# Optimization experiments

Hardware: AMD Instinct MI355X
Metric: run time of the kernel (lower is better)

The kernel has to match this reference:

```python
import jax, jax.numpy as jnp
import numpy as np

N = 30000   # nodes
E = 120000  # edges
G = 512     # graphs in batch
F_IN = 1
H1 = 32
H2 = 64
NC = 10


def _lin_init(key, fan_in, fan_out):
    s = 1.0 / np.sqrt(fan_in)
    kw, kb = jax.random.split(key)
    w = jax.random.uniform(kw, (fan_in, fan_out), jnp.float32, minval=-s, maxval=s)
    b = jax.random.uniform(kb, (fan_out,), jnp.float32, minval=-s, maxval=s)
    return w, b


def setup_inputs() -> dict:
    key = jax.random.key(0)
    ks = jax.random.split(key, 16)
    inp = {}
    inp["x"] = jax.random.normal(ks[0], (N, F_IN), jnp.float32)
    inp["edge_attr"] = jax.random.uniform(ks[1], (E, 2), jnp.float32)
    inp["pos"] = jax.random.uniform(ks[2], (N, 2), jnp.float32) * 27.0
    inp["w1a"], inp["b1a"] = _lin_init(ks[3], 2, 25)
    inp["w1b"], inp["b1b"] = _lin_init(ks[4], 25, F_IN * H1)
    inp["root1"], inp["bias1"] = _lin_init(ks[5], F_IN, H1)
    inp["w2a"], inp["b2a"] = _lin_init(ks[6], 2, 25)
    inp["w2b"], inp["b2b"] = _lin_init(ks[7], 25, H1 * H2)
    inp["root2"], inp["bias2"] = _lin_init(ks[8], H1, H2)
    inp["fc1_w"], inp["fc1_b"] = _lin_init(ks[9], H2, 128)
    inp["fc2_w"], inp["fc2_b"] = _lin_init(ks[10], 128, NC)
    inp["edge_index"] = jax.random.randint(ks[11], (2, E), 0, N)
    inp["batch"] = jnp.sort(jax.random.randint(ks[12], (N,), 0, G))
    return inp


def _seg_mean(v, idx, n):
    s = jax.ops.segment_sum(v, idx, num_segments=n)
    c = jax.ops.segment_sum(jnp.ones((v.shape[0], 1), v.dtype), idx, num_segments=n)
    return s / jnp.maximum(c, 1.0)


def _nnconv(x, src, dst, ea, wa, ba, wb, bb, root, bias, n_seg, n_out):
    # per-edge weight matrix from edge MLP: [E, f_in, f_out]
    f_in, f_out = root.shape
    W = (jax.nn.relu(ea @ wa + ba) @ wb + bb).reshape(-1, f_in, f_out)
    msg = jnp.einsum('ei,eio->eo', x[src], W)          # gather + per-edge matmul
    aggr = _seg_mean(msg, dst, n_seg)[:n_out]          # mean scatter-reduce
    return aggr + x @ root + bias


def _forward(x, edge_attr, pos, w1a, b1a, w1b, b1b, root1, bias1,
             w2a, b2a, w2b, b2b, root2, bias2, fc1_w, fc1_b, fc2_w, fc2_b,
             edge_index, batch):
    row, col = edge_index[0], edge_index[1]
    h = jax.nn.elu(_nnconv(x, row, col, edge_attr, w1a, b1a, w1b, b1b,
                           root1, bias1, N, N))
    # graclus stand-in: fixed pairwise matching (consecutive cluster ids)
    n2 = N // 2
    cluster1 = jnp.arange(N) // 2
    x2 = jax.ops.segment_max(h, cluster1, num_segments=n2)     # max_pool x
    pos2 = _seg_mean(pos, cluster1, n2)                        # pool_pos (mean)
    batch2 = batch[0::2]                                       # pool_batch via perm
    row2 = cluster1[row]
    col2 = cluster1[col]
    mask = row2 != col2                                        # drop self loops
    col2m = jnp.where(mask, col2, n2)                          # route to dummy seg
    cart = (pos2[col2] - pos2[row2]) * mask[:, None]           # cartesian pseudo
    max_v = jnp.abs(cart).max()
    ea2 = cart / (2.0 * max_v) + 0.5
    h2 = jax.nn.elu(_nnconv(x2, row2, col2m, ea2, w2a, b2a, w2b, b2b,
                            root2, bias2, n2 + 1, n2))
    n3 = n2 // 2
    cluster2 = jnp.arange(n2) // 2
    x3 = jax.ops.segment_max(h2, cluster2, num_segments=n3)    # max_pool_x
    batch3 = batch2[0::2]
    g = _seg_mean(x3, batch3, G)                               # global_mean_pool
    g = jax.nn.elu(g @ fc1_w + fc1_b)                          # dropout off (eval)
    return jax.nn.log_softmax(g @ fc2_w + fc2_b, axis=1)


def reference(x, edge_attr, pos, w1a, b1a, w1b, b1b, root1, bias1,
              w2a, b2a, w2b, b2b, root2, bias2, fc1_w, fc1_b, fc2_w, fc2_b,
              edge_index, batch):
    return _forward(x, edge_attr, pos, w1a, b1a, w1b, b1b, root1, bias1,
                    w2a, b2a, w2b, b2b, root2, bias2, fc1_w, fc1_b,
                    fc2_w, fc2_b, edge_index, batch)
```

## Files before the change

kernel.cpp:

```cpp
#include <hip/hip_runtime.h>
#include <hip/hip_bf16.h>

#define N_NODES 30000
#define N_EDGES 120000
#define NGRAPH  512
#define N2      15000
#define N3      7500
#define NC      10

#define TSN   4
#define NTS   (N2 / TSN)
#define EC4   64
#define NB1   32
#define NBLK1 ((N_NODES + NB1 - 1) / NB1)
#define EC1   128

#define SC_C1 118
#define SC_C2 59
#define SC_CS 15
#define SC_CT (SC_C1 + SC_C2 + SC_CS)

typedef __hip_bfloat16 bf16;

__device__ __forceinline__ float lo(const float* p, int i) { return p[i]; }
__device__ __forceinline__ float lo(const bf16* p, int i) { return __bfloat162float(p[i]); }
__device__ __forceinline__ void sto(float* p, int i, float v) { p[i] = v; }
__device__ __forceinline__ void sto(bf16* p, int i, float v) { p[i] = __float2bfloat16(v); }
__device__ __forceinline__ float elu(float x) { return x > 0.f ? x : expm1f(x); }
template <typename T> __host__ __device__ constexpr int want_flag() { return sizeof(T) == 4 ? 1 : 0; }

#define MV_OFF    0
#define GS_OFF    1
#define GC_OFF    32769
#define DEG1_OFF  33281
#define DEG2_OFF  63281
#define DEGS_OFF  78281
#define ZERO_FLOATS 82031
#define OFF1_OFF  82031
#define CUR1_OFF  112032
#define OFF2_OFF  142032
#define CUR2_OFF  157033
#define OFFS_OFF  172033
#define CURS_OFF  175784
#define BSUM_OFF  179534
#define ES1_OFF   179726
#define ESS_OFF   299726
#define DPOS_OFF  419726
#define X2_OFF    539726
#define P2_OFF    1019726
#define CT_OFF    1049726
#define H2_OFF    1289726
#define MSG_OFF   2249726
#define FLAG_OFF  9929726

__global__ __launch_bounds__(256) void k0_detect(const void* x, const void* ea, int* flag) {
  const bf16* xb = (const bf16*)x;
  const bf16* eb = (const bf16*)ea;
  int tid = threadIdx.x;
  float a = __bfloat162float(xb[tid]);
  float b = __bfloat162float(eb[tid]);
  int bad = (!(fabsf(a) < 1e3f)) || (!(fabsf(b) < 1e3f));
  unsigned long long m = __ballot(bad);
  __shared__ int anyb[4];
  int w = tid >> 6;
  if ((tid & 63) == 0) anyb[w] = (m != 0ULL) ? 1 : 0;
  __syncthreads();
  if (tid == 0) flag[0] = (anyb[0] | anyb[1] | anyb[2] | anyb[3]);
}

__global__ __launch_bounds__(256) void kc_deg(const int* __restrict__ ei,
                                              int* __restrict__ deg1,
                                              int* __restrict__ deg2,
                                              int* __restrict__ degS) {
  int e = blockIdx.x * 256 + threadIdx.x;
  if (e >= N_EDGES) return;
  int row = ei[e], col = ei[N_EDGES + e];
  atomicAdd(deg1 + col, 1);
  int r2 = row >> 1, c2 = col >> 1;
  if (r2 != c2) {
    atomicAdd(deg2 + c2, 1);
    atomicAdd(degS + (r2 >> 2), 1);
  }
}

__global__ __launch_bounds__(256) void ks_scanA(
    const int* __restrict__ deg1, const int* __restrict__ deg2, const int* __restrict__ degS,
    int* __restrict__ off1, int* __restrict__ off2, int* __restrict__ offS,
    int* __restrict__ bsum) {
  __shared__ int buf[256];
  int c = blockIdx.x, tid = threadIdx.x;
  const int* deg; int* off; int n, local;
  if (c < SC_C1)              { deg = deg1; off = off1; n = 30000; local = c; }
  else if (c < SC_C1 + SC_C2) { deg = deg2; off = off2; n = 15000; local = c - SC_C1; }
  else                        { deg = degS; off = offS; n = 3750;  local = c - SC_C1 - SC_C2; }
  int i = local * 256 + tid;
  int v = (i < n) ? deg[i] : 0;
  buf[tid] = v;
  __syncthreads();
  for (int s = 1; s < 256; s <<= 1) {
    int t = (tid >= s) ? buf[tid - s] : 0;
    __syncthreads();
    buf[tid] += t;
    __syncthreads();
  }
  if (i <= n) off[i] = buf[tid] - v;
  if (tid == 255) bsum[c] = buf[255];
}

__global__ __launch_bounds__(256) void ks_scanB(int* __restrict__ bsum) {
  __shared__ int buf[256];
  int a = blockIdx.x, tid = threadIdx.x;
  int nc, cb;
  if (a == 0)      { nc = SC_C1; cb = 0; }
  else if (a == 1) { nc = SC_C2; cb = SC_C1; }
  else             { nc = SC_CS; cb = SC_C1 + SC_C2; }
  int v = (tid < nc) ? bsum[cb + tid] : 0;
  buf[tid] = v;
  __syncthreads();
  for (int s = 1; s < 256; s <<= 1) {
    int t = (tid >= s) ? buf[tid - s] : 0;
    __syncthreads();
    buf[tid] += t;
    __syncthreads();
  }
  if (tid < nc) bsum[cb + tid] = buf[tid] - v;
}

__global__ __launch_bounds__(256) void ks_scanC(
    int* __restrict__ off1, int* __restrict__ off2, int* __restrict__ offS,
    int* __restrict__ cur1, int* __restrict__ cur2, int* __restrict__ curS,
    const int* __restrict__ bsum) {
  int c = blockIdx.x, tid = threadIdx.x;
  int* off; int* cur; int n, local;
  if (c < SC_C1)              { off = off1; cur = cur1; n = 30000; local = c; }
  else if (c < SC_C1 + SC_C2) { off = off2; cur = cur2; n = 15000; local = c - SC_C1; }
  else                        { off = offS; cur = curS; n = 3750;  local = c - SC_C1 - SC_C2; }
  int add = bsum[c];
  int i = local * 256 + tid;
  if (i <= n) off[i] += add;
  if (i < n) cur[i] = off[i];
}

__global__ __launch_bounds__(256) void kc_place(const int* __restrict__ ei,
                                                int* __restrict__ cur1, int* __restrict__ es1,
                                                int* __restrict__ cur2, int* __restrict__ dpos,
                                                int* __restrict__ curS, int* __restrict__ ess) {
  int e = blockIdx.x * 256 + threadIdx.x;
  if (e >= N_EDGES) return;
  int row = ei[e], col = ei[N_EDGES + e];
  int p = atomicAdd(cur1 + col, 1);
  es1[p] = e;
  int r2 = row >> 1, c2 = col >> 1;
  if (r2 != c2) {
    int q = atomicAdd(cur2 + c2, 1);
    dpos[e] = q;
    int u = atomicAdd(curS + (r2 >> 2), 1);
    ess[u] = e;
  }
}

template <typename T>
__global__ __launch_bounds__(256, 4) void k1_blk(
    const int* __restrict__ flag,
    const T* __restrict__ x, const T* __restrict__ ea, const T* __restrict__ pos,
    const int* __restrict__ ei,
    const T* __restrict__ w1a, const T* __restrict__ b1a,
    const T* __restrict__ w1b, const T* __restrict__ b1b,
    const T* __restrict__ root1, const T* __restrict__ bias1,
    const int* __restrict__ off1, const int* __restrict__ es1,
    float* __restrict__ x2, float* __restrict__ pos2) {
  if (flag[0] != want_flag<T>()) return;
  __shared__ float w1a_l[50];
  __shared__ float b1a_l[25];
  __shared__ float w1b_l[800];
  __shared__ float b1b_l[32];
  __shared__ float r1_l[32];
  __shared__ float bs1_l[32];
  __shared__ float tl2[25][EC1];
  __shared__ float xsl[EC1];
  __shared__ float hbuf[NB1][33];
  __shared__ int offl[NB1 + 1];
  int tid = threadIdx.x, t = blockIdx.x;
  int n0 = t * NB1;
  for (int j = tid; j < 50; j += 256) w1a_l[j] = lo(w1a, j);
  for (int j = tid; j < 25; j += 256) b1a_l[j] = lo(b1a, j);
  for (int j = tid; j < 800; j += 256) w1b_l[j] = lo(w1b, j);
  if (tid < 32) {
    b1b_l[tid] = lo(b1b, tid);
    r1_l[tid] = lo(root1, tid);
    bs1_l[tid] = lo(bias1, tid);
  }
  if (tid <= NB1) {
    int n = n0 + tid; if (n > N_NODES) n = N_NODES;
    offl[tid] = off1[n];
  }
  __syncthreads();
  int jbeg = offl[0], jend = offl[NB1];
  int wv = tid >> 6, lane = tid & 63, o = lane & 31, hf = lane >> 5;
  float acc[8];
#pragma unroll
  for (int s = 0; s < 8; ++s) acc[s] = 0.f;
  for (int jb = jbeg; jb < jend; jb += EC1) {
    int ecnt = jend - jb; if (ecnt > EC1) ecnt = EC1;
    __syncthreads();
    if (tid < ecnt) {
      int e = es1[jb + tid];
      float a0 = lo(ea, 2 * e), a1 = lo(ea, 2 * e + 1);
      xsl[tid] = lo(x, ei[e]);
#pragma unroll
      for (int k = 0; k < 25; ++k)
        tl2[k][tid] = fmaxf(a0 * w1a_l[k] + a1 * w1a_l[25 + k] + b1a_l[k], 0.f);
    }
    __syncthreads();
#pragma unroll
    for (int s = 0; s < 8; ++s) {
      int nl = wv + 4 * s;
      int lj = offl[nl]; if (lj < jb) lj = jb;
      int hj = offl[nl + 1]; if (hj > jb + ecnt) hj = jb + ecnt;
      for (int j = lj + hf; j < hj; j += 2) {
        int sj = j - jb;
        float macc = b1b_l[o];
#pragma unroll
        for (int k = 0; k < 25; ++k) macc += tl2[k][sj] * w1b_l[k * 32 + o];
        acc[s] += xsl[sj] * macc;
      }
    }
  }
#pragma unroll
  for (int s = 0; s < 8; ++s) {
    int nl = wv + 4 * s;
    float a = acc[s] + __shfl_xor(acc[s], 32, 64);
    int n = n0 + nl;
    if (hf == 0 && n < N_NODES) {
      float c = (float)(offl[nl + 1] - offl[nl]);
      c = fmaxf(c, 1.f);
      hbuf[nl][o] = elu(a / c + lo(x, n) * r1_l[o] + bs1_l[o]);
    }
  }
  __syncthreads();
  for (int idx = tid; idx < (NB1 / 2) * 32; idx += 256) {
    int pl = idx >> 5, oo = idx & 31;
    int m = t * (NB1 / 2) + pl;
    if (m < N2)
      x2[m * 32 + oo] = fmaxf(hbuf[2 * pl][oo], hbuf[2 * pl + 1][oo]);
  }
  if (tid < NB1) {
    int pl = tid >> 1, c = tid & 1;
    int m = t * (NB1 / 2) + pl;
    if (m < N2)
      pos2[m * 2 + c] = 0.5f * (lo(pos, (2 * m) * 2 + c) + lo(pos, (2 * m + 1) * 2 + c));
  }
}

__global__ __launch_bounds__(256) void k3_cart(
    const int* __restrict__ ei, const float* __restrict__ pos2,
    float* __restrict__ cart, unsigned int* __restrict__ maxv) {
  int e = blockIdx.x * 256 + threadIdx.x;
  float m = 0.f;
  if (e < N_EDGES) {
    int r2 = ei[e] >> 1, c2 = ei[N_EDGES + e] >> 1;
    float cx = 0.f, cy = 0.f;
    if (r2 != c2) {
      cx = pos2[2 * c2] - pos2[2 * r2];
      cy = pos2[2 * c2 + 1] - pos2[2 * r2 + 1];
    }
    cart[2 * e] = cx;
    cart[2 * e + 1] = cy;
    m = fmaxf(fabsf(cx), fabsf(cy));
  }
#pragma unroll
  for (int s = 32; s > 0; s >>= 1)
    m = fmaxf(m, __shfl_xor(m, s, 64));
  __shared__ float wm[4];
  int lane = threadIdx.x & 63, wid = threadIdx.x >> 6;
  if (lane == 0) wm[wid] = m;
  __syncthreads();
  if (threadIdx.x == 0) {
    float mm = fmaxf(fmaxf(wm[0], wm[1]), fmaxf(wm[2], wm[3]));
    atomicMax(maxv, __float_as_uint(mm));
  }
}

template <typename T>
__global__ __launch_bounds__(256, 3) void k4_src(
    const int* __restrict__ flag,
    const int* __restrict__ ei, const float* __restrict__ cart, const float* __restrict__ maxv_f,
    const float* __restrict__ x2,
    const T* __restrict__ w2a, const T* __restrict__ b2a,
    const T* __restrict__ w2b, const T* __restrict__ b2b,
    const int* __restrict__ offS, const int* __restrict__ ess,
    const int* __restrict__ dpos,
    float* __restrict__ msg) {
  if (flag[0] != want_flag<T>()) return;
  __shared__ float Y[TSN][26][64];
  __shared__ float xl[TSN][32];
  __shared__ float w2a_l[50];
  __shared__ float b2a_l[25];
  __shared__ __align__(16) float tl[EC4][28];
  __shared__ int dpl[EC4];
  __shared__ int nll[EC4];
  __shared__ float axl[EC4], ayl[EC4];
  int tid = threadIdx.x, t = blockIdx.x;
  int n0 = t * TSN;
  if (tid < TSN * 32) xl[tid >> 5][tid & 31] = x2[n0 * 32 + tid];
  for (int j = tid; j < 50; j += 256) w2a_l[j] = lo(w2a, j);
  for (int j = tid; j < 25; j += 256) b2a_l[j] = lo(b2a, j);
  __syncthreads();
  int w = tid >> 6, o = tid & 63;
  for (int kk = w; kk < 26; kk += 4) {
    const T* srcp = (kk < 25) ? (w2b + kk * 2048) : b2b;
    float a0 = 0.f, a1 = 0.f, a2 = 0.f, a3 = 0.f;
#pragma unroll 8
    for (int i = 0; i < 32; ++i) {
      float q = lo(srcp, i * 64 + o);
      a0 += xl[0][i] * q;
      a1 += xl[1][i] * q;
      a2 += xl[2][i] * q;
      a3 += xl[3][i] * q;
    }
    Y[0][kk][o] = a0; Y[1][kk][o] = a1; Y[2][kk][o] = a2; Y[3][kk][o] = a3;
  }
  float inv = 0.5f / maxv_f[0];
  int j0 = offS[t], j1 = offS[t + 1];
  for (int jb = j0; jb < j1; jb += EC4) {
    int ecnt = j1 - jb; if (ecnt > EC4) ecnt = EC4;
    __syncthreads();
    if (tid < ecnt) {
      int e = ess[jb + tid];
      int r2 = ei[e] >> 1;
      nll[tid] = r2 & (TSN - 1);
      dpl[tid] = dpos[e];
      axl[tid] = cart[2 * e] * inv + 0.5f;
      ayl[tid] = cart[2 * e + 1] * inv + 0.5f;
    }
    __syncthreads();
    for (int idx = tid; idx < ecnt * 32; idx += 256) {
      int j = idx >> 5, k = idx & 31;
      if (k < 25)
        tl[j][k] = fmaxf(axl[j] * w2a_l[k] + ayl[j] * w2a_l[25 + k] + b2a_l[k], 0.f);
    }
    __syncthreads();
    for (int j = w; j < ecnt; j += 4) {
      const float* Yp = &Y[nll[j]][0][0];
      const float* tp = tl[j];
      float acc0 = Yp[25 * 64 + o], acc1 = 0.f, acc2 = 0.f, acc3 = 0.f;
#pragma unroll
      for (int k = 0; k < 24; k += 4) {
        acc0 += tp[k]     * Yp[k * 64 + o];
        acc1 += tp[k + 1] * Yp[(k + 1) * 64 + o];
        acc2 += tp[k + 2] * Yp[(k + 2) * 64 + o];
        acc3 += tp[k + 3] * Yp[(k + 3) * 64 + o];
      }
      acc0 += tp[24] * Yp[24 * 64 + o];
      msg[(size_t)dpl[j] * 64 + o] = (acc0 + acc1) + (acc2 + acc3);
    }
  }
}

template <typename T>
__global__ __launch_bounds__(256) void k5_gather(
    const int* __restrict__ flag,
    const float* __restrict__ msg, const int* __restrict__ off2,
    const float* __restrict__ x2,
    const T* __restrict__ root2, const T* __restrict__ bias2,
    float* __restrict__ h2) {
  if (flag[0] != want_flag<T>()) return;
  __shared__ float r2_l[2048];
  __shared__ float b2_l[64];
  int tid = threadIdx.x;
  for (int j = tid; j < 2048; j += 256) r2_l[j] = lo(root2, j);
  if (tid < 64) b2_l[tid] = lo(bias2, tid);
  __syncthreads();
  int d = blockIdx.x * 4 + (tid >> 6);
  int o = tid & 63;
  int j0 = off2[d], j1 = off2[d + 1];
  float s0 = 0.f, s1 = 0.f;
  int j = j0;
  for (; j + 1 < j1; j += 2) {
    s0 += msg[(size_t)j * 64 + o];
    s1 += msg[(size_t)(j + 1) * 64 + o];
  }
  if (j < j1) s0 += msg[(size_t)j * 64 + o];
  float c = fmaxf((float)(j1 - j0), 1.f);
  float r = b2_l[o];
  const float* xr = x2 + d * 32;
#pragma unroll 8
  for (int i = 0; i < 32; ++i) r += xr[i] * r2_l[i * 64 + o];
  h2[d * 64 + o] = elu((s0 + s1) / c + r);
}

#define K6CH 16
__global__ __launch_bounds__(256) void k6_pool2(
    const float* __restrict__ h2, const int* __restrict__ batch,
    float* __restrict__ gsum, float* __restrict__ gcnt) {
  int wid = blockIdx.x * 4 + (threadIdx.x >> 6);
  int lane = threadIdx.x & 63;
  int m0 = wid * K6CH;
  if (m0 >= N3) return;
  int m1 = m0 + K6CH < N3 ? m0 + K6CH : N3;
  int bcur = batch[4 * m0];
  float acc = 0.f, cnt = 0.f;
  for (int m = m0; m < m1; ++m) {
    int b = batch[4 * m];
    float v = fmaxf(h2[(2 * m) * 64 + lane], h2[(2 * m + 1) * 64 + lane]);
    if (b != bcur) {
      atomicAdd(gsum + bcur * 64 + lane, acc);
      if (lane == 0) atomicAdd(gcnt + bcur, cnt);
      acc = 0.f; cnt = 0.f; bcur = b;
    }
    acc += v; cnt += 1.f;
  }
  atomicAdd(gsum + bcur * 64 + lane, acc);
  if (lane == 0) atomicAdd(gcnt + bcur, cnt);
}

template <typename T>
__global__ __launch_bounds__(128) void k7_head(
    const int* __restrict__ flag,
    const float* __restrict__ gsum, const float* __restrict__ gcnt,
    const T* __restrict__ fc1_w, const T* __restrict__ fc1_b,
    const T* __restrict__ fc2_w, const T* __restrict__ fc2_b,
    T* __restrict__ out) {
  if (flag[0] != want_flag<T>()) return;
  __shared__ float gv[64];
  __shared__ float h1s[128];
  __shared__ float zs[NC];
  __shared__ float lse;
  int g = blockIdx.x, tid = threadIdx.x;
  if (tid < 64) gv[tid] = gsum[g * 64 + tid] / fmaxf(gcnt[g], 1.f);
  __syncthreads();
  float a = lo(fc1_b, tid);
#pragma unroll 8
  for (int o = 0; o < 64; ++o) a += gv[o] * lo(fc1_w, o * 128 + tid);
  h1s[tid] = elu(a);
  __syncthreads();
  if (tid < NC) {
    float s = lo(fc2_b, tid);
    for (int j = 0; j < 128; ++j) s += h1s[j] * lo(fc2_w, j * NC + tid);
    zs[tid] = s;
  }
  __syncthreads();
  if (tid == 0) {
    float m = -1e30f;
    for (int c = 0; c < NC; ++c) m = fmaxf(m, zs[c]);
    float s = 0.f;
    for (int c = 0; c < NC; ++c) s += expf(zs[c] - m);
    lse = m + logf(s);
  }
  __syncthreads();
  if (tid < NC) sto(out, g * NC + tid, zs[tid] - lse);
}

template <typename T>
static void run_conv1(void* const* d_in, float* ws, hipStream_t stream) {
  const int* ei   = (const int*)d_in[19];
  const int* flag = (const int*)(ws + FLAG_OFF);
  k1_blk<T><<<NBLK1, 256, 0, stream>>>(
      flag, (const T*)d_in[0], (const T*)d_in[1], (const T*)d_in[2], ei,
      (const T*)d_in[3], (const T*)d_in[4], (const T*)d_in[5], (const T*)d_in[6],
      (const T*)d_in[7], (const T*)d_in[8],
      (const int*)(ws + OFF1_OFF), (const int*)(ws + ES1_OFF),
      ws + X2_OFF, ws + P2_OFF);
}

template <typename T>
static void run_conv2(void* const* d_in, float* ws, hipStream_t stream) {
  const int* ei   = (const int*)d_in[19];
  const int* flag = (const int*)(ws + FLAG_OFF);
  k4_src<T><<<NTS, 256, 0, stream>>>(
      flag, ei, ws + CT_OFF, ws + MV_OFF, ws + X2_OFF,
      (const T*)d_in[9], (const T*)d_in[10], (const T*)d_in[11], (const T*)d_in[12],
      (const int*)(ws + OFFS_OFF), (const int*)(ws + ESS_OFF),
      (const int*)(ws + DPOS_OFF), ws + MSG_OFF);
  k5_gather<T><<<N2 / 4, 256, 0, stream>>>(
      flag, ws + MSG_OFF, (const int*)(ws + OFF2_OFF), ws + X2_OFF,
      (const T*)d_in[13], (const T*)d_in[14], ws + H2_OFF);
}

extern "C" void kernel_launch(void* const* d_in, const int* in_sizes, int n_in,
                              void* d_out, int out_size, void* d_ws, size_t ws_size,
                              hipStream_t stream) {
  float* ws = (float*)d_ws;
  const int* flag = (const int*)(ws + FLAG_OFF);
  const int* ei = (const int*)d_in[19];
  const int* batch = (const int*)d_in[20];

  k0_detect<<<1, 256, 0, stream>>>(d_in[0], d_in[1], (int*)(ws + FLAG_OFF));
  hipMemsetAsync(d_ws, 0, (size_t)ZERO_FLOATS * 4, stream);

  kc_deg<<<(N_EDGES + 255) / 256, 256, 0, stream>>>(
      ei, (int*)(ws + DEG1_OFF), (int*)(ws + DEG2_OFF), (int*)(ws + DEGS_OFF));
  ks_scanA<<<SC_CT, 256, 0, stream>>>(
      (const int*)(ws + DEG1_OFF), (const int*)(ws + DEG2_OFF), (const int*)(ws + DEGS_OFF),
      (int*)(ws + OFF1_OFF), (int*)(ws + OFF2_OFF), (int*)(ws + OFFS_OFF),
      (int*)(ws + BSUM_OFF));
  ks_scanB<<<3, 256, 0, stream>>>((int*)(ws + BSUM_OFF));
  ks_scanC<<<SC_CT, 256, 0, stream>>>(
      (int*)(ws + OFF1_OFF), (int*)(ws + OFF2_OFF), (int*)(ws + OFFS_OFF),
      (int*)(ws + CUR1_OFF), (int*)(ws + CUR2_OFF), (int*)(ws + CURS_OFF),
      (const int*)(ws + BSUM_OFF));
  kc_place<<<(N_EDGES + 255) / 256, 256, 0, stream>>>(
      ei, (int*)(ws + CUR1_OFF), (int*)(ws + ES1_OFF),
      (int*)(ws + CUR2_OFF), (int*)(ws + DPOS_OFF),
      (int*)(ws + CURS_OFF), (int*)(ws + ESS_OFF));

  run_conv1<float>(d_in, ws, stream);
  run_conv1<bf16>(d_in, ws, stream);

  k3_cart<<<(N_EDGES + 255) / 256, 256, 0, stream>>>(
      ei, ws + P2_OFF, ws + CT_OFF, (unsigned int*)(ws + MV_OFF));

  run_conv2<float>(d_in, ws, stream);
  run_conv2<bf16>(d_in, ws, stream);

  k6_pool2<<<(N3 / K6CH + 4) / 4, 256, 0, stream>>>(
      ws + H2_OFF, batch, ws + GS_OFF, ws + GC_OFF);
  k7_head<float><<<NGRAPH, 128, 0, stream>>>(
      flag, ws + GS_OFF, ws + GC_OFF,
      (const float*)d_in[15], (const float*)d_in[16],
      (const float*)d_in[17], (const float*)d_in[18], (float*)d_out);
  k7_head<bf16><<<NGRAPH, 128, 0, stream>>>(
      flag, ws + GS_OFF, ws + GC_OFF,
      (const bf16*)d_in[15], (const bf16*)d_in[16],
      (const bf16*)d_in[17], (const bf16*)d_in[18], (bf16*)d_out);
}
```

Before: 283.6 us.

## Merge dtype-specialized kernels, fuse pooling into conv2 gather, vectorize per-edge matmuls

```diff
diff --git a/kernel.cpp b/kernel.cpp
--- a/kernel.cpp
+++ b/kernel.cpp
@@ -14,6 +14,7 @@
 #define NB1   32
 #define NBLK1 ((N_NODES + NB1 - 1) / NB1)
 #define EC1   128
+#define NDEGB ((N_EDGES + 255) / 256)
 
 #define SC_C1 118
 #define SC_C2 59
@@ -27,7 +28,6 @@
 __device__ __forceinline__ void sto(float* p, int i, float v) { p[i] = v; }
 __device__ __forceinline__ void sto(bf16* p, int i, float v) { p[i] = __float2bfloat16(v); }
 __device__ __forceinline__ float elu(float x) { return x > 0.f ? x : expm1f(x); }
-template <typename T> __host__ __device__ constexpr int want_flag() { return sizeof(T) == 4 ? 1 : 0; }
 
 #define MV_OFF    0
 #define GS_OFF    1
@@ -49,29 +49,57 @@
 #define X2_OFF    539726
 #define P2_OFF    1019726
 #define CT_OFF    1049726
-#define H2_OFF    1289726
-#define MSG_OFF   2249726
-#define FLAG_OFF  9929726
-
-__global__ __launch_bounds__(256) void k0_detect(const void* x, const void* ea, int* flag) {
-  const bf16* xb = (const bf16*)x;
-  const bf16* eb = (const bf16*)ea;
-  int tid = threadIdx.x;
-  float a = __bfloat162float(xb[tid]);
-  float b = __bfloat162float(eb[tid]);
-  int bad = (!(fabsf(a) < 1e3f)) || (!(fabsf(b) < 1e3f));
-  unsigned long long m = __ballot(bad);
-  __shared__ int anyb[4];
-  int w = tid >> 6;
-  if ((tid & 63) == 0) anyb[w] = (m != 0ULL) ? 1 : 0;
-  __syncthreads();
-  if (tid == 0) flag[0] = (anyb[0] | anyb[1] | anyb[2] | anyb[3]);
-}
-
-__global__ __launch_bounds__(256) void kc_deg(const int* __restrict__ ei,
-                                              int* __restrict__ deg1,
-                                              int* __restrict__ deg2,
-                                              int* __restrict__ degS) {
+#define MSG_OFF   1289726
+#define FLAG_OFF  8969726
+
+struct K1Smem {
+  float tl2[EC1][28];
+  float axl[EC1], ayl[EC1];
+  float xsl[EC1];
+  float w1a[50];
+  float b1a[25];
+  float b1b[32];
+  float r1[32];
+  float bs1[32];
+  float hbuf[NB1][33];
+  int offl[NB1 + 1];
+};
+
+struct K4Smem {
+  float YT[TSN][64][36];
+  float tl[EC4][28];
+  float xl[TSN][32];
+  float w2a[50];
+  float b2a[25];
+  float axl[EC4], ayl[EC4];
+  int dpl[EC4];
+  int nll[EC4];
+};
+
+struct K5Smem {
+  float r2l[2048];
+  float b2l[64];
+  float hl[4][64];
+};
+
+__global__ __launch_bounds__(256) void kc_deg(
+    const int* __restrict__ ei, const void* x, const void* ea, int* __restrict__ flag,
+    int* __restrict__ deg1, int* __restrict__ deg2, int* __restrict__ degS) {
+  if (blockIdx.x == NDEGB) {
+    const bf16* xb = (const bf16*)x;
+    const bf16* eb = (const bf16*)ea;
+    int tid = threadIdx.x;
+    float a = __bfloat162float(xb[tid]);
+    float b = __bfloat162float(eb[tid]);
+    int bad = (!(fabsf(a) < 1e3f)) || (!(fabsf(b) < 1e3f));
+    unsigned long long m = __ballot(bad);
+    __shared__ int anyb[4];
+    int w = tid >> 6;
+    if ((tid & 63) == 0) anyb[w] = (m != 0ULL) ? 1 : 0;
+    __syncthreads();
+    if (tid == 0) flag[0] = (anyb[0] | anyb[1] | anyb[2] | anyb[3]);
+    return;
+  }
   int e = blockIdx.x * 256 + threadIdx.x;
   if (e >= N_EDGES) return;
   int row = ei[e], col = ei[N_EDGES + e];
@@ -160,8 +188,7 @@
 }
 
 template <typename T>
-__global__ __launch_bounds__(256, 4) void k1_blk(
-    const int* __restrict__ flag,
+__device__ void k1_impl(K1Smem& S,
     const T* __restrict__ x, const T* __restrict__ ea, const T* __restrict__ pos,
     const int* __restrict__ ei,
     const T* __restrict__ w1a, const T* __restrict__ b1a,
@@ -169,34 +196,27 @@
     const T* __restrict__ root1, const T* __restrict__ bias1,
     const int* __restrict__ off1, const int* __restrict__ es1,
     float* __restrict__ x2, float* __restrict__ pos2) {
-  if (flag[0] != want_flag<T>()) return;
-  __shared__ float w1a_l[50];
-  __shared__ float b1a_l[25];
-  __shared__ float w1b_l[800];
-  __shared__ float b1b_l[32];
-  __shared__ float r1_l[32];
-  __shared__ float bs1_l[32];
-  __shared__ float tl2[25][EC1];
-  __shared__ float xsl[EC1];
-  __shared__ float hbuf[NB1][33];
-  __shared__ int offl[NB1 + 1];
   int tid = threadIdx.x, t = blockIdx.x;
   int n0 = t * NB1;
-  for (int j = tid; j < 50; j += 256) w1a_l[j] = lo(w1a, j);
-  for (int j = tid; j < 25; j += 256) b1a_l[j] = lo(b1a, j);
-  for (int j = tid; j < 800; j += 256) w1b_l[j] = lo(w1b, j);
+  for (int j = tid; j < 50; j += 256) S.w1a[j] = lo(w1a, j);
+  for (int j = tid; j < 25; j += 256) S.b1a[j] = lo(b1a, j);
   if (tid < 32) {
-    b1b_l[tid] = lo(b1b, tid);
-    r1_l[tid] = lo(root1, tid);
-    bs1_l[tid] = lo(bias1, tid);
+    S.b1b[tid] = lo(b1b, tid);
+    S.r1[tid] = lo(root1, tid);
+    S.bs1[tid] = lo(bias1, tid);
   }
   if (tid <= NB1) {
     int n = n0 + tid; if (n > N_NODES) n = N_NODES;
-    offl[tid] = off1[n];
-  }
-  __syncthreads();
-  int jbeg = offl[0], jend = offl[NB1];
+    S.offl[tid] = off1[n];
+  }
   int wv = tid >> 6, lane = tid & 63, o = lane & 31, hf = lane >> 5;
+  float wreg[28];
+#pragma unroll
+  for (int k = 0; k < 25; ++k) wreg[k] = lo(w1b, k * 32 + o);
+  wreg[25] = wreg[26] = wreg[27] = 0.f;
+  __syncthreads();
+  int jbeg = S.offl[0], jend = S.offl[NB1];
+  float bb = S.b1b[o];
   float acc[8];
 #pragma unroll
   for (int s = 0; s < 8; ++s) acc[s] = 0.f;
@@ -205,24 +225,37 @@
     __syncthreads();
     if (tid < ecnt) {
       int e = es1[jb + tid];
-      float a0 = lo(ea, 2 * e), a1 = lo(ea, 2 * e + 1);
-      xsl[tid] = lo(x, ei[e]);
-#pragma unroll
-      for (int k = 0; k < 25; ++k)
-        tl2[k][tid] = fmaxf(a0 * w1a_l[k] + a1 * w1a_l[25 + k] + b1a_l[k], 0.f);
+      S.axl[tid] = lo(ea, 2 * e);
+      S.ayl[tid] = lo(ea, 2 * e + 1);
+      S.xsl[tid] = lo(x, ei[e]);
+    }
+    __syncthreads();
+    for (int idx = tid; idx < ecnt * 32; idx += 256) {
+      int j = idx >> 5, k = idx & 31;
+      if (k < 25)
+        S.tl2[j][k] = fmaxf(S.axl[j] * S.w1a[k] + S.ayl[j] * S.w1a[25 + k] + S.b1a[k], 0.f);
+      else if (k < 28)
+        S.tl2[j][k] = 0.f;
     }
     __syncthreads();
 #pragma unroll
     for (int s = 0; s < 8; ++s) {
       int nl = wv + 4 * s;
-      int lj = offl[nl]; if (lj < jb) lj = jb;
-      int hj = offl[nl + 1]; if (hj > jb + ecnt) hj = jb + ecnt;
+      int lj = S.offl[nl]; if (lj < jb) lj = jb;
+      int hj = S.offl[nl + 1]; if (hj > jb + ecnt) hj = jb + ecnt;
       for (int j = lj + hf; j < hj; j += 2) {
         int sj = j - jb;
-        float macc = b1b_l[o];
-#pragma unroll
-        for (int k = 0; k < 25; ++k) macc += tl2[k][sj] * w1b_l[k * 32 + o];
-        acc[s] += xsl[sj] * macc;
+        const float4* tq4 = (const float4*)S.tl2[sj];
+        float m0 = bb, m1 = 0.f, m2 = 0.f, m3 = 0.f;
+#pragma unroll
+        for (int q = 0; q < 7; ++q) {
+          float4 tv = tq4[q];
+          m0 += tv.x * wreg[4 * q];
+          m1 += tv.y * wreg[4 * q + 1];
+          m2 += tv.z * wreg[4 * q + 2];
+          m3 += tv.w * wreg[4 * q + 3];
+        }
+        acc[s] += S.xsl[sj] * ((m0 + m1) + (m2 + m3));
       }
     }
   }
@@ -232,9 +265,9 @@
     float a = acc[s] + __shfl_xor(acc[s], 32, 64);
     int n = n0 + nl;
     if (hf == 0 && n < N_NODES) {
-      float c = (float)(offl[nl + 1] - offl[nl]);
+      float c = (float)(S.offl[nl + 1] - S.offl[nl]);
       c = fmaxf(c, 1.f);
-      hbuf[nl][o] = elu(a / c + lo(x, n) * r1_l[o] + bs1_l[o]);
+      S.hbuf[nl][o] = elu(a / c + lo(x, n) * S.r1[o] + S.bs1[o]);
     }
   }
   __syncthreads();
@@ -242,7 +275,7 @@
     int pl = idx >> 5, oo = idx & 31;
     int m = t * (NB1 / 2) + pl;
     if (m < N2)
-      x2[m * 32 + oo] = fmaxf(hbuf[2 * pl][oo], hbuf[2 * pl + 1][oo]);
+      x2[m * 32 + oo] = fmaxf(S.hbuf[2 * pl][oo], S.hbuf[2 * pl + 1][oo]);
   }
   if (tid < NB1) {
     int pl = tid >> 1, c = tid & 1;
@@ -250,6 +283,24 @@
     if (m < N2)
       pos2[m * 2 + c] = 0.5f * (lo(pos, (2 * m) * 2 + c) + lo(pos, (2 * m + 1) * 2 + c));
   }
+}
+
+__global__ __launch_bounds__(256, 4) void k1_both(
+    const int* __restrict__ flag,
+    const void* x, const void* ea, const void* pos, const int* ei,
+    const void* w1a, const void* b1a, const void* w1b, const void* b1b,
+    const void* root1, const void* bias1,
+    const int* off1, const int* es1, float* x2, float* pos2) {
+  extern __shared__ char sm1[];
+  K1Smem& S = *reinterpret_cast<K1Smem*>(sm1);
+  if (flag[0] == 1)
+    k1_impl<float>(S, (const float*)x, (const float*)ea, (const float*)pos, ei,
+                   (const float*)w1a, (const float*)b1a, (const float*)w1b, (const float*)b1b,
+                   (const float*)root1, (const float*)bias1, off1, es1, x2, pos2);
+  else
+    k1_impl<bf16>(S, (const bf16*)x, (const bf16*)ea, (const bf16*)pos, ei,
+                  (const bf16*)w1a, (const bf16*)b1a, (const bf16*)w1b, (const bf16*)b1b,
+                  (const bf16*)root1, (const bf16*)bias1, off1, es1, x2, pos2);
 }
 
 __global__ __launch_bounds__(256) void k3_cart(
@@ -282,43 +333,35 @@
 }
 
 template <typename T>
-__global__ __launch_bounds__(256, 3) void k4_src(
-    const int* __restrict__ flag,
+__device__ void k4_impl(K4Smem& S,
     const int* __restrict__ ei, const float* __restrict__ cart, const float* __restrict__ maxv_f,
     const float* __restrict__ x2,
     const T* __restrict__ w2a, const T* __restrict__ b2a,
     const T* __restrict__ w2b, const T* __restrict__ b2b,
     const int* __restrict__ offS, const int* __restrict__ ess,
-    const int* __restrict__ dpos,
-    float* __restrict__ msg) {
-  if (flag[0] != want_flag<T>()) return;
-  __shared__ float Y[TSN][26][64];
-  __shared__ float xl[TSN][32];
-  __shared__ float w2a_l[50];
-  __shared__ float b2a_l[25];
-  __shared__ __align__(16) float tl[EC4][28];
-  __shared__ int dpl[EC4];
-  __shared__ int nll[EC4];
-  __shared__ float axl[EC4], ayl[EC4];
+    const int* __restrict__ dpos, float* __restrict__ msg) {
   int tid = threadIdx.x, t = blockIdx.x;
   int n0 = t * TSN;
-  if (tid < TSN * 32) xl[tid >> 5][tid & 31] = x2[n0 * 32 + tid];
-  for (int j = tid; j < 50; j += 256) w2a_l[j] = lo(w2a, j);
-  for (int j = tid; j < 25; j += 256) b2a_l[j] = lo(b2a, j);
+  if (tid < TSN * 32) S.xl[tid >> 5][tid & 31] = x2[n0 * 32 + tid];
+  for (int j = tid; j < 50; j += 256) S.w2a[j] = lo(w2a, j);
+  for (int j = tid; j < 25; j += 256) S.b2a[j] = lo(b2a, j);
   __syncthreads();
   int w = tid >> 6, o = tid & 63;
-  for (int kk = w; kk < 26; kk += 4) {
-    const T* srcp = (kk < 25) ? (w2b + kk * 2048) : b2b;
+  for (int kk = w; kk < 28; kk += 4) {
     float a0 = 0.f, a1 = 0.f, a2 = 0.f, a3 = 0.f;
+    if (kk < 26) {
+      const T* srcp = (kk < 25) ? (w2b + kk * 2048) : b2b;
 #pragma unroll 8
-    for (int i = 0; i < 32; ++i) {
-      float q = lo(srcp, i * 64 + o);
-      a0 += xl[0][i] * q;
-      a1 += xl[1][i] * q;
-      a2 += xl[2][i] * q;
-      a3 += xl[3][i] * q;
-    }
-    Y[0][kk][o] = a0; Y[1][kk][o] = a1; Y[2][kk][o] = a2; Y[3][kk][o] = a3;
+      for (int i = 0; i < 32; ++i) {
+        float q = lo(srcp, i * 64 + o);
+        a0 += S.xl[0][i] * q;
+        a1 += S.xl[1][i] * q;
+        a2 += S.xl[2][i] * q;
+        a3 += S.xl[3][i] * q;
+      }
+    }
+    S.YT[0][o][kk] = a0; S.YT[1][o][kk] = a1;
+    S.YT[2][o][kk] = a2; S.YT[3][o][kk] = a3;
   }
   float inv = 0.5f / maxv_f[0];
   int j0 = offS[t], j1 = offS[t + 1];
@@ -328,51 +371,63 @@
     if (tid < ecnt) {
       int e = ess[jb + tid];
       int r2 = ei[e] >> 1;
-      nll[tid] = r2 & (TSN - 1);
-      dpl[tid] = dpos[e];
-      axl[tid] = cart[2 * e] * inv + 0.5f;
-      ayl[tid] = cart[2 * e + 1] * inv + 0.5f;
+      S.nll[tid] = r2 & (TSN - 1);
+      S.dpl[tid] = dpos[e];
+      S.axl[tid] = cart[2 * e] * inv + 0.5f;
+      S.ayl[tid] = cart[2 * e + 1] * inv + 0.5f;
     }
     __syncthreads();
     for (int idx = tid; idx < ecnt * 32; idx += 256) {
       int j = idx >> 5, k = idx & 31;
       if (k < 25)
-        tl[j][k] = fmaxf(axl[j] * w2a_l[k] + ayl[j] * w2a_l[25 + k] + b2a_l[k], 0.f);
+        S.tl[j][k] = fmaxf(S.axl[j] * S.w2a[k] + S.ayl[j] * S.w2a[25 + k] + S.b2a[k], 0.f);
+      else if (k < 28)
+        S.tl[j][k] = (k == 25) ? 1.f : 0.f;
     }
     __syncthreads();
     for (int j = w; j < ecnt; j += 4) {
-      const float* Yp = &Y[nll[j]][0][0];
-      const float* tp = tl[j];
-      float acc0 = Yp[25 * 64 + o], acc1 = 0.f, acc2 = 0.f, acc3 = 0.f;
-#pragma unroll
-      for (int k = 0; k < 24; k += 4) {
-        acc0 += tp[k]     * Yp[k * 64 + o];
-        acc1 += tp[k + 1] * Yp[(k + 1) * 64 + o];
-        acc2 += tp[k + 2] * Yp[(k + 2) * 64 + o];
-        acc3 += tp[k + 3] * Yp[(k + 3) * 64 + o];
+      const float4* yq = (const float4*)&S.YT[S.nll[j]][o][0];
+      const float4* tq = (const float4*)S.tl[j];
+      float a0 = 0.f, a1 = 0.f, a2 = 0.f, a3 = 0.f;
+#pragma unroll
+      for (int q = 0; q < 7; ++q) {
+        float4 tv = tq[q], yv = yq[q];
+        a0 += tv.x * yv.x; a1 += tv.y * yv.y;
+        a2 += tv.z * yv.z; a3 += tv.w * yv.w;
       }
-      acc0 += tp[24] * Yp[24 * 64 + o];
-      msg[(size_t)dpl[j] * 64 + o] = (acc0 + acc1) + (acc2 + acc3);
-    }
-  }
+      msg[(size_t)S.dpl[j] * 64 + o] = (a0 + a1) + (a2 + a3);
+    }
+  }
+}
+
+__global__ __launch_bounds__(256, 3) void k4_both(
+    const int* __restrict__ flag,
+    const int* ei, const float* cart, const float* maxv_f, const float* x2,
+    const void* w2a, const void* b2a, const void* w2b, const void* b2b,
+    const int* offS, const int* ess, const int* dpos, float* msg) {
+  extern __shared__ char sm4[];
+  K4Smem& S = *reinterpret_cast<K4Smem*>(sm4);
+  if (flag[0] == 1)
+    k4_impl<float>(S, ei, cart, maxv_f, x2, (const float*)w2a, (const float*)b2a,
+                   (const float*)w2b, (const float*)b2b, offS, ess, dpos, msg);
+  else
+    k4_impl<bf16>(S, ei, cart, maxv_f, x2, (const bf16*)w2a, (const bf16*)b2a,
+                  (const bf16*)w2b, (const bf16*)b2b, offS, ess, dpos, msg);
 }
 
 template <typename T>
-__global__ __launch_bounds__(256) void k5_gather(
-    const int* __restrict__ flag,
+__device__ void k5_impl(K5Smem& S,
     const float* __restrict__ msg, const int* __restrict__ off2,
     const float* __restrict__ x2,
     const T* __restrict__ root2, const T* __restrict__ bias2,
-    float* __restrict__ h2) {
-  if (flag[0] != want_flag<T>()) return;
-  __shared__ float r2_l[2048];
-  __shared__ float b2_l[64];
+    const int* __restrict__ batch,
+    float* __restrict__ gsum, float* __restrict__ gcnt) {
   int tid = threadIdx.x;
-  for (int j = tid; j < 2048; j += 256) r2_l[j] = lo(root2, j);
-  if (tid < 64) b2_l[tid] = lo(bias2, tid);
-  __syncthreads();
-  int d = blockIdx.x * 4 + (tid >> 6);
-  int o = tid & 63;
+  for (int j = tid; j < 2048; j += 256) S.r2l[j] = lo(root2, j);
+  if (tid < 64) S.b2l[tid] = lo(bias2, tid);
+  __syncthreads();
+  int w = tid >> 6, o = tid & 63;
+  int d = blockIdx.x * 4 + w;
   int j0 = off2[d], j1 = off2[d + 1];
   float s0 = 0.f, s1 = 0.f;
   int j = j0;
@@ -382,46 +437,40 @@
   }
   if (j < j1) s0 += msg[(size_t)j * 64 + o];
   float c = fmaxf((float)(j1 - j0), 1.f);
-  float r = b2_l[o];
+  float r = S.b2l[o];
   const float* xr = x2 + d * 32;
 #pragma unroll 8
-  for (int i = 0; i < 32; ++i) r += xr[i] * r2_l[i * 64 + o];
-  h2[d * 64 + o] = elu((s0 + s1) / c + r);
-}
-
-#define K6CH 16
-__global__ __launch_bounds__(256) void k6_pool2(
-    const float* __restrict__ h2, const int* __restrict__ batch,
-    float* __restrict__ gsum, float* __restrict__ gcnt) {
-  int wid = blockIdx.x * 4 + (threadIdx.x >> 6);
-  int lane = threadIdx.x & 63;
-  int m0 = wid * K6CH;
-  if (m0 >= N3) return;
-  int m1 = m0 + K6CH < N3 ? m0 + K6CH : N3;
-  int bcur = batch[4 * m0];
-  float acc = 0.f, cnt = 0.f;
-  for (int m = m0; m < m1; ++m) {
-    int b = batch[4 * m];
-    float v = fmaxf(h2[(2 * m) * 64 + lane], h2[(2 * m + 1) * 64 + lane]);
-    if (b != bcur) {
-      atomicAdd(gsum + bcur * 64 + lane, acc);
-      if (lane == 0) atomicAdd(gcnt + bcur, cnt);
-      acc = 0.f; cnt = 0.f; bcur = b;
-    }
-    acc += v; cnt += 1.f;
-  }
-  atomicAdd(gsum + bcur * 64 + lane, acc);
-  if (lane == 0) atomicAdd(gcnt + bcur, cnt);
+  for (int i = 0; i < 32; ++i) r += xr[i] * S.r2l[i * 64 + o];
+  S.hl[w][o] = elu((s0 + s1) / c + r);
+  __syncthreads();
+  if (tid < 128) {
+    int p = tid >> 6, oo = tid & 63;
+    float v = fmaxf(S.hl[2 * p][oo], S.hl[2 * p + 1][oo]);
+    int m = blockIdx.x * 2 + p;
+    int g = batch[4 * m];
+    atomicAdd(gsum + g * 64 + oo, v);
+    if (oo == 0) atomicAdd(gcnt + g, 1.f);
+  }
+}
+
+__global__ __launch_bounds__(256) void k5_both(
+    const int* __restrict__ flag,
+    const float* msg, const int* off2, const float* x2,
+    const void* root2, const void* bias2, const int* batch,
+    float* gsum, float* gcnt) {
+  extern __shared__ char sm5[];
+  K5Smem& S = *reinterpret_cast<K5Smem*>(sm5);
+  if (flag[0] == 1)
+    k5_impl<float>(S, msg, off2, x2, (const float*)root2, (const float*)bias2, batch, gsum, gcnt);
+  else
+    k5_impl<bf16>(S, msg, off2, x2, (const bf16*)root2, (const bf16*)bias2, batch, gsum, gcnt);
 }
 
 template <typename T>
-__global__ __launch_bounds__(128) void k7_head(
-    const int* __restrict__ flag,
-    const float* __restrict__ gsum, const float* __restrict__ gcnt,
-    const T* __restrict__ fc1_w, const T* __restrict__ fc1_b,
-    const T* __restrict__ fc2_w, const T* __restrict__ fc2_b,
-    T* __restrict__ out) {
-  if (flag[0] != want_flag<T>()) return;
+__device__ void k7_impl(const float* __restrict__ gsum, const float* __restrict__ gcnt,
+                        const T* __restrict__ fc1_w, const T* __restrict__ fc1_b,
+                        const T* __restrict__ fc2_w, const T* __restrict__ fc2_b,
+                        T* __restrict__ out) {
   __shared__ float gv[64];
   __shared__ float h1s[128];
   __shared__ float zs[NC];
@@ -451,30 +500,17 @@
   if (tid < NC) sto(out, g * NC + tid, zs[tid] - lse);
 }
 
-template <typename T>
-static void run_conv1(void* const* d_in, float* ws, hipStream_t stream) {
-  const int* ei   = (const int*)d_in[19];
-  const int* flag = (const int*)(ws + FLAG_OFF);
-  k1_blk<T><<<NBLK1, 256, 0, stream>>>(
-      flag, (const T*)d_in[0], (const T*)d_in[1], (const T*)d_in[2], ei,
-      (const T*)d_in[3], (const T*)d_in[4], (const T*)d_in[5], (const T*)d_in[6],
-      (const T*)d_in[7], (const T*)d_in[8],
-      (const int*)(ws + OFF1_OFF), (const int*)(ws + ES1_OFF),
-      ws + X2_OFF, ws + P2_OFF);
-}
-
-template <typename T>
-static void run_conv2(void* const* d_in, float* ws, hipStream_t stream) {
-  const int* ei   = (const int*)d_in[19];
-  const int* flag = (const int*)(ws + FLAG_OFF);
-  k4_src<T><<<NTS, 256, 0, stream>>>(
-      flag, ei, ws + CT_OFF, ws + MV_OFF, ws + X2_OFF,
-      (const T*)d_in[9], (const T*)d_in[10], (const T*)d_in[11], (const T*)d_in[12],
-      (const int*)(ws + OFFS_OFF), (const int*)(ws + ESS_OFF),
-      (const int*)(ws + DPOS_OFF), ws + MSG_OFF);
-  k5_gather<T><<<N2 / 4, 256, 0, stream>>>(
-      flag, ws + MSG_OFF, (const int*)(ws + OFF2_OFF), ws + X2_OFF,
-      (const T*)d_in[13], (const T*)d_in[14], ws + H2_OFF);
+__global__ __launch_bounds__(128) void k7_both(
+    const int* __restrict__ flag,
+    const float* gsum, const float* gcnt,
+    const void* fc1_w, const void* fc1_b, const void* fc2_w, const void* fc2_b,
+    void* out) {
+  if (flag[0] == 1)
+    k7_impl<float>(gsum, gcnt, (const float*)fc1_w, (const float*)fc1_b,
+                   (const float*)fc2_w, (const float*)fc2_b, (float*)out);
+  else
+    k7_impl<bf16>(gsum, gcnt, (const bf16*)fc1_w, (const bf16*)fc1_b,
+                  (const bf16*)fc2_w, (const bf16*)fc2_b, (bf16*)out);
 }
 
 extern "C" void kernel_launch(void* const* d_in, const int* in_sizes, int n_in,
@@ -485,11 +521,11 @@
   const int* ei = (const int*)d_in[19];
   const int* batch = (const int*)d_in[20];
 
-  k0_detect<<<1, 256, 0, stream>>>(d_in[0], d_in[1], (int*)(ws + FLAG_OFF));
   hipMemsetAsync(d_ws, 0, (size_t)ZERO_FLOATS * 4, stream);
 
-  kc_deg<<<(N_EDGES + 255) / 256, 256, 0, stream>>>(
-      ei, (int*)(ws + DEG1_OFF), (int*)(ws + DEG2_OFF), (int*)(ws + DEGS_OFF));
+  kc_deg<<<NDEGB + 1, 256, 0, stream>>>(
+      ei, d_in[0], d_in[1], (int*)(ws + FLAG_OFF),
+      (int*)(ws + DEG1_OFF), (int*)(ws + DEG2_OFF), (int*)(ws + DEGS_OFF));
   ks_scanA<<<SC_CT, 256, 0, stream>>>(
       (const int*)(ws + DEG1_OFF), (const int*)(ws + DEG2_OFF), (const int*)(ws + DEGS_OFF),
       (int*)(ws + OFF1_OFF), (int*)(ws + OFF2_OFF), (int*)(ws + OFFS_OFF),
@@ -499,28 +535,31 @@
       (int*)(ws + OFF1_OFF), (int*)(ws + OFF2_OFF), (int*)(ws + OFFS_OFF),
       (int*)(ws + CUR1_OFF), (int*)(ws + CUR2_OFF), (int*)(ws + CURS_OFF),
       (const int*)(ws + BSUM_OFF));
-  kc_place<<<(N_EDGES + 255) / 256, 256, 0, stream>>>(
+  kc_place<<<NDEGB, 256, 0, stream>>>(
       ei, (int*)(ws + CUR1_OFF), (int*)(ws + ES1_OFF),
       (int*)(ws + CUR2_OFF), (int*)(ws + DPOS_OFF),
       (int*)(ws + CURS_OFF), (int*)(ws + ESS_OFF));
 
-  run_conv1<float>(d_in, ws, stream);
-  run_conv1<bf16>(d_in, ws, stream);
-
-  k3_cart<<<(N_EDGES + 255) / 256, 256, 0, stream>>>(
+  k1_both<<<NBLK1, 256, sizeof(K1Smem), stream>>>(
+      flag, d_in[0], d_in[1], d_in[2], ei,
+      d_in[3], d_in[4], d_in[5], d_in[6], d_in[7], d_in[8],
+      (const int*)(ws + OFF1_OFF), (const int*)(ws + ES1_OFF),
+      ws + X2_OFF, ws + P2_OFF);
+
+  k3_cart<<<NDEGB, 256, 0, stream>>>(
       ei, ws + P2_OFF, ws + CT_OFF, (unsigned int*)(ws + MV_OFF));
 
-  run_conv2<float>(d_in, ws, stream);
-  run_conv2<bf16>(d_in, ws, stream);
-
-  k6_pool2<<<(N3 / K6CH + 4) / 4, 256, 0, stream>>>(
-      ws + H2_OFF, batch, ws + GS_OFF, ws + GC_OFF);
-  k7_head<float><<<NGRAPH, 128, 0, stream>>>(
+  k4_both<<<NTS, 256, sizeof(K4Smem), stream>>>(
+      flag, ei, ws + CT_OFF, ws + MV_OFF, ws + X2_OFF,
+      d_in[9], d_in[10], d_in[11], d_in[12],
+      (const int*)(ws + OFFS_OFF), (const int*)(ws + ESS_OFF),
+      (const int*)(ws + DPOS_OFF), ws + MSG_OFF);
+
+  k5_both<<<N2 / 4, 256, sizeof(K5Smem), stream>>>(
+      flag, ws + MSG_OFF, (const int*)(ws + OFF2_OFF), ws + X2_OFF,
+      d_in[13], d_in[14], batch, ws + GS_OFF, ws + GC_OFF);
+
+  k7_both<<<NGRAPH, 128, 0, stream>>>(
       flag, ws + GS_OFF, ws + GC_OFF,
-      (const float*)d_in[15], (const float*)d_in[16],
-      (const float*)d_in[17], (const float*)d_in[18], (float*)d_out);
-  k7_head<bf16><<<NGRAPH, 128, 0, stream>>>(
-      flag, ws + GS_OFF, ws + GC_OFF,
-      (const bf16*)d_in[15], (const bf16*)d_in[16],
-      (const bf16*)d_in[17], (const bf16*)d_in[18], (bf16*)d_out);
-}
+      d_in[15], d_in[16], d_in[17], d_in[18], d_out);
+}
```

Measured after the change: 294.2 us. 3.7% more time.
